# Performance work log

Hardware: AMD Instinct MI355X
Metric: run time of the kernel (lower is better)

Reference implementation:

```python
import jax, jax.numpy as jnp
import numpy as np

N = 32          # agents_num
IN_DIM = 16     # node feature dim (excluding 2 pos cols)
HID = 128
HEADS = 4
OUT = 5
DUEL_H = 256
RADIUS = 0.3
LATENT = HID + HID * HEADS * 2  # 1152
BS = 128


def _lin(k, i, o):
    s = 1.0 / np.sqrt(i)
    return jax.random.uniform(k, (i, o), minval=-s, maxval=s, dtype=jnp.float32)


def setup_inputs() -> dict:
    key = jax.random.key(0)
    ks = jax.random.split(key, 16)
    pos = jax.random.uniform(ks[0], (BS, N, 2))
    feats = jax.random.normal(ks[1], (BS, N, IN_DIM))
    aidx = jax.random.randint(ks[2], (BS,), 0, N).astype(jnp.float32)
    node = jnp.concatenate([pos, feats], axis=-1).reshape(BS, N * (2 + IN_DIM))
    obs = jnp.concatenate([node, aidx[:, None]], axis=1)  # (BS, N*(2+IN_DIM)+1)
    return {
        "obs": obs,
        "enc_w1": _lin(ks[3], IN_DIM, HID), "enc_b1": jnp.zeros((HID,)),
        "enc_w2": _lin(ks[4], HID, HID), "enc_b2": jnp.zeros((HID,)),
        "wl1": _lin(ks[5], HID, HEADS * HID), "wr1": _lin(ks[6], HID, HEADS * HID),
        "att1": jax.random.normal(ks[7], (HEADS, HID)) * 0.1, "bias1": jnp.zeros((HEADS * HID,)),
        "wl2": _lin(ks[8], HID * HEADS, HEADS * HID), "wr2": _lin(ks[9], HID * HEADS, HEADS * HID),
        "att2": jax.random.normal(ks[10], (HEADS, HID)) * 0.1, "bias2": jnp.zeros((HEADS * HID,)),
        "q_w1": _lin(ks[11], LATENT, DUEL_H), "q_b1": jnp.zeros((DUEL_H,)),
        "q_w2": _lin(ks[12], DUEL_H, OUT), "q_b2": jnp.zeros((OUT,)),
        "v_w1": _lin(ks[13], LATENT, DUEL_H), "v_b1": jnp.zeros((DUEL_H,)),
        "v_w2": _lin(ks[14], DUEL_H, 1), "v_b2": jnp.zeros((1,)),
    }


def _gatv2(x, adj, wl, wr, att, bias):
    # Dense-masked GATv2 (PyG semantics: lin_l on source j, lin_r on target i,
    # leaky_relu(x_i + x_j) . att, softmax over neighbors j, aggregate lin_l(x_j)).
    bs, n, _ = x.shape
    gl = (x @ wl).reshape(bs, n, HEADS, HID)  # source transform
    gr = (x @ wr).reshape(bs, n, HEADS, HID)  # target transform
    e = jax.nn.leaky_relu(gr[:, :, None] + gl[:, None, :], 0.2)  # [b, i, j, h, c]
    logits = jnp.einsum('bijhc,hc->bijh', e, att)
    logits = jnp.where(adj[..., None], logits, -jnp.inf)  # diag always True (self loops)
    alpha = jax.nn.softmax(logits, axis=2)
    out = jnp.einsum('bijh,bjhc->bihc', alpha, gl).reshape(bs, n, HEADS * HID)
    return out + bias


def reference(obs, enc_w1, enc_b1, enc_w2, enc_b2,
              wl1, wr1, att1, bias1, wl2, wr2, att2, bias2,
              q_w1, q_b1, q_w2, q_b2, v_w1, v_b1, v_w2, v_b2):
    bs = obs.shape[0]
    node = obs[:, :-1].reshape(bs, N, 2 + IN_DIM)
    pos, feats = node[..., :2], node[..., 2:]
    aidx = jnp.clip(obs[:, -1], 0, N - 1).astype(jnp.int32)

    # radius_graph (per-graph, loop=False) + GATv2 add_self_loops => diag True
    d2 = jnp.sum((pos[:, :, None] - pos[:, None, :]) ** 2, axis=-1)  # [bs, N, N]
    adj = (d2 < RADIUS ** 2) | jnp.eye(N, dtype=bool)

    # encoder MLP then ReLU (as in forward)
    h = jax.nn.relu(feats @ enc_w1 + enc_b1)
    x = jax.nn.relu(h @ enc_w2 + enc_b2)  # [bs, N, HID]

    b = jnp.arange(bs)
    x1 = x[b, aidx]  # [bs, HID]

    x = jax.nn.relu(_gatv2(x, adj, wl1, wr1, att1, bias1))  # [bs, N, HID*HEADS]
    x2 = x[b, aidx]

    x = jax.nn.relu(_gatv2(x, adj, wl2, wr2, att2, bias2))
    x3 = x[b, aidx]

    x_cat = jnp.concatenate([x1, x2, x3], axis=1)  # [bs, LATENT]

    q = jax.nn.relu(x_cat @ q_w1 + q_b1) @ q_w2 + q_b2  # [bs, OUT]
    v = jax.nn.relu(x_cat @ v_w1 + v_b1) @ v_w2 + v_b2  # [bs, 1]
    return q - q.mean(axis=1, keepdims=True) + v
```

## Files before the change

kernel.cpp:

```cpp
#include <hip/hip_runtime.h>
#include <hip/hip_bf16.h>

typedef unsigned int uint_t;
typedef unsigned short ushort_t;
typedef __attribute__((ext_vector_type(8))) short short8;
typedef __attribute__((ext_vector_type(4))) float floatx4;

__device__ __forceinline__ float4 fma4(float4 a, float s, float4 w){
  a.x += s*w.x; a.y += s*w.y; a.z += s*w.z; a.w += s*w.w; return a;
}
__device__ __forceinline__ float4 relu4(float4 a){
  return make_float4(fmaxf(a.x,0.f),fmaxf(a.y,0.f),fmaxf(a.z,0.f),fmaxf(a.w,0.f));
}
__device__ __forceinline__ unsigned bf16rne(float f){
  unsigned u = __float_as_uint(f);
  return (u + 0x7fffu + ((u>>16)&1u)) >> 16;
}
__device__ __forceinline__ uint_t packbf(float f){
  unsigned hb = bf16rne(f);
  float hf = __uint_as_float(hb<<16);
  unsigned lb = bf16rne(f - hf);
  return (hb<<16) | lb;
}
__device__ __forceinline__ uint4 pack4(float4 v){
  uint4 u; u.x=packbf(v.x); u.y=packbf(v.y); u.z=packbf(v.z); u.w=packbf(v.w); return u;
}
__device__ __forceinline__ float unpk(uint_t u){
  return __uint_as_float(u & 0xffff0000u) + __uint_as_float(u<<16);
}
#define UNPACK8(u0,u1,hi,lo) \
  hi[0]=(short)(u0.x>>16); lo[0]=(short)u0.x; \
  hi[1]=(short)(u0.y>>16); lo[1]=(short)u0.y; \
  hi[2]=(short)(u0.z>>16); lo[2]=(short)u0.z; \
  hi[3]=(short)(u0.w>>16); lo[3]=(short)u0.w; \
  hi[4]=(short)(u1.x>>16); lo[4]=(short)u1.x; \
  hi[5]=(short)(u1.y>>16); lo[5]=(short)u1.y; \
  hi[6]=(short)(u1.z>>16); lo[6]=(short)u1.z; \
  hi[7]=(short)(u1.w>>16); lo[7]=(short)u1.w;


__device__ __forceinline__ void hgemm_body(
    const uint_t* __restrict__ xcatpk,
    const ushort_t* __restrict__ qw1Thi, const ushort_t* __restrict__ qw1Tlo,
    const ushort_t* __restrict__ vw1Thi, const ushort_t* __restrict__ vw1Tlo,
    float* __restrict__ part, int ks, int ct, int t)
{
  const int w = t>>6, lane = t&63, m = lane&15, quad = lane>>4;
  const ushort_t* Bhi = (ct<4) ? qw1Thi : vw1Thi;
  const int cbl = (ct<4) ? ct*64 : (ct-4)*64;
  const int cbg = (ct<4) ? ct*64 : 256 + (ct-4)*64;
  const uint_t* ap = xcatpk + (size_t)w*18432 + m*32 + quad*8 + (size_t)(ks*5)*512;
  const ushort_t* bp0 = Bhi + (size_t)((cbl>>4)+0)*18432 + m*32 + quad*8 + (size_t)(ks*5)*512;
  const ushort_t* bp1 = Bhi + (size_t)((cbl>>4)+1)*18432 + m*32 + quad*8 + (size_t)(ks*5)*512;
  const ushort_t* bp2 = Bhi + (size_t)((cbl>>4)+2)*18432 + m*32 + quad*8 + (size_t)(ks*5)*512;
  const ushort_t* bp3 = Bhi + (size_t)((cbl>>4)+3)*18432 + m*32 + quad*8 + (size_t)(ks*5)*512;
  const size_t lod = (size_t)(qw1Tlo - qw1Thi);
  floatx4 acc[4];
  #pragma unroll
  for (int i=0;i<4;i++) acc[i] = (floatx4){0.f,0.f,0.f,0.f};
  #pragma unroll
  for (int kc=0; kc<5; kc++){
    const uint4 ua0 = *(const uint4*)(ap);
    const uint4 ua1 = *(const uint4*)(ap+4);
    ap += 512;
    short8 ahi, alo;
    UNPACK8(ua0,ua1,ahi,alo)
    const ushort_t* bps[4] = {bp0, bp1, bp2, bp3};
    #pragma unroll
    for (int nt=0; nt<4; nt++){
      const short8 bh = *(const short8*)(bps[nt] + kc*512);
      const short8 bl = *(const short8*)(bps[nt] + kc*512 + lod);
      acc[nt] = __builtin_amdgcn_mfma_f32_16x16x32_bf16(ahi, bh, acc[nt], 0,0,0);
      acc[nt] = __builtin_amdgcn_mfma_f32_16x16x32_bf16(ahi, bl, acc[nt], 0,0,0);
      acc[nt] = __builtin_amdgcn_mfma_f32_16x16x32_bf16(alo, bh, acc[nt], 0,0,0);
    }
  }
  float* pdst = part + (size_t)ks*65536;
  const int crow0 = w*16 + quad*4;
  #pragma unroll
  for (int nt=0; nt<4; nt++){
    const int col = cbg + nt*16 + m;
    #pragma unroll
    for (int r=0;r<4;r++)
      pdst[(size_t)(crow0 + r)*512 + col] = acc[nt][r];
  }
}

__global__ __launch_bounds__(256) void prep_kernel(
    const float* __restrict__ obs,
    const float* __restrict__ enc_w1, const float* __restrict__ enc_b1,
    const float* __restrict__ enc_w2, const float* __restrict__ enc_b2,
    const float* __restrict__ wl1, const float* __restrict__ wr1,
    ushort_t* __restrict__ wl1Thi, ushort_t* __restrict__ wl1Tlo,
    ushort_t* __restrict__ wr1Thi, ushort_t* __restrict__ wr1Tlo,
    uint_t* __restrict__ xpk, uint_t* __restrict__ xcatpk,
    unsigned* __restrict__ adjw, int* __restrict__ aiw)
{
  const int t = threadIdx.x, bid = blockIdx.x;
  if (bid >= 512){
    __shared__ float sm[32][33];
    const int cw = bid - 512;
    const float* in; ushort_t* ohi; ushort_t* olo; int tt;
    const int K = 128, N = 512;
    if (cw < 64){ in=wl1; ohi=wl1Thi; olo=wl1Tlo; tt=cw; }
    else        { in=wr1; ohi=wr1Thi; olo=wr1Tlo; tt=cw-64; }
    const int ktiles = K>>5;
    const int kt = tt % ktiles, nt = tt / ktiles;
    const int r = t>>5, c = t&31;
    #pragma unroll
    for (int i=0;i<4;i++)
      sm[r+i*8][c] = in[(size_t)(kt*32 + r + i*8)*N + nt*32 + c];
    __syncthreads();
    #pragma unroll
    for (int i=0;i<4;i++){
      const int nl = r + i*8;
      const int n  = nt*32 + nl;
      const float f = sm[c][nl];
      const unsigned hb = bf16rne(f);
      const float hf = __uint_as_float(hb<<16);
      const unsigned lb = bf16rne(f - hf);
      const size_t off = (size_t)(n>>4)*(16*K) + (size_t)kt*512 + (size_t)(n&15)*32 + c;
      ohi[off] = (ushort_t)hb;
      olo[off] = (ushort_t)lb;
    }
    return;
  }
  __shared__ float s_pos[64];
  __shared__ float s_feats[128];
  __shared__ __align__(16) float s_h[8*132];
  __shared__ int s_ai;
  const int s = bid & 127, g = bid >> 7;
  const float* ob = obs + s*577;

  if (t==0){
    float a = ob[576];
    a = fminf(fmaxf(a, 0.f), 31.f);
    s_ai = (int)a;
    if (g==0) aiw[s] = (int)a;
  }
  if (t < 128){ const int n=t>>4, f=t&15; s_feats[t] = ob[(g*8+n)*18+2+f]; }
  if (g==0 && t>=128 && t<192){ const int u=t-128; s_pos[u] = ob[(u>>1)*18 + (u&1)]; }
  __syncthreads();

  if (g==0 && t < 32){
    const float px = s_pos[2*t], py = s_pos[2*t+1];
    const float R2 = 0.09f;
    unsigned mm = 0u;
    for (int j=0;j<32;j++){
      const float dx = __fsub_rn(px, s_pos[2*j]), dy = __fsub_rn(py, s_pos[2*j+1]);
      const float d2 = __fadd_rn(__fmul_rn(dx,dx), __fmul_rn(dy,dy));
      if (d2 <= R2 || j==t) mm |= (1u<<j);
    }
    adjw[s*32+t] = mm;
  }

  const int n = t>>5, c0 = (t&31)*4;
  {
    float4 a = *(const float4*)(enc_b1+c0);
    #pragma unroll
    for (int f=0; f<16; f++)
      a = fma4(a, s_feats[n*16+f], *(const float4*)(enc_w1 + f*128 + c0));
    *(float4*)&s_h[n*132+c0] = relu4(a);
  }
  __syncthreads();
  {
    float4 a = *(const float4*)(enc_b2+c0);
    for (int k=0;k<128;k+=4){
      const float4 hv = *(const float4*)&s_h[n*132+k];
      a = fma4(a, hv.x, *(const float4*)(enc_w2 + (k+0)*128 + c0));
      a = fma4(a, hv.y, *(const float4*)(enc_w2 + (k+1)*128 + c0));
      a = fma4(a, hv.z, *(const float4*)(enc_w2 + (k+2)*128 + c0));
      a = fma4(a, hv.w, *(const float4*)(enc_w2 + (k+3)*128 + c0));
    }
    a = relu4(a);
    const uint4 p = pack4(a);
    const int i = g*8 + n;
    uint_t* xp = xpk + (size_t)(s*2 + (i>>4))*2048 + (c0>>5)*512 + (i&15)*32 + (c0&31);
    *(uint4*)xp = p;
    if (i == s_ai){
      uint_t* xc = xcatpk + (size_t)(s>>4)*18432 + (c0>>5)*512 + (s&15)*32 + (c0&31);
      *(uint4*)xc = p;
    }
  }
}

__global__ __launch_bounds__(512) void pa1_kernel(
    const uint_t* __restrict__ xpk,
    const ushort_t* __restrict__ wl1Thi, const ushort_t* __restrict__ wl1Tlo,
    const ushort_t* __restrict__ wr1Thi, const ushort_t* __restrict__ wr1Tlo,
    const float* __restrict__ att, const float* __restrict__ bias,
    const unsigned* __restrict__ adjw, const int* __restrict__ aiw,
    const float* __restrict__ wl2, const float* __restrict__ q_w1, const float* __restrict__ v_w1,
    ushort_t* __restrict__ wl2Thi, ushort_t* __restrict__ wl2Tlo,
    ushort_t* __restrict__ qw1Thi, ushort_t* __restrict__ qw1Tlo,
    ushort_t* __restrict__ vw1Thi, ushort_t* __restrict__ vw1Tlo,
    uint_t* __restrict__ x2pk, uint_t* __restrict__ xcatpk)
{
  __shared__ __align__(16) float s_gl[32*132];
  __shared__ __align__(16) float s_glB[32*132];
  __shared__ __align__(16) float s_gr[32*132];
  __shared__ __align__(16) float s_grB[32*132];
  __shared__ __align__(16) float s_att[128];
  __shared__ __align__(16) float s_b[128];
  __shared__ float s_lg[32*33];
  __shared__ unsigned s_adj[32];
  const int t = threadIdx.x, bid = blockIdx.x;

  if (bid >= 512){
    const int cw = bid - 512;
    const float* in; ushort_t* ohi; ushort_t* olo; int K, N, tt;
    if (cw < 256)      { in=wl2;  ohi=wl2Thi; olo=wl2Tlo; K=512;  N=512; tt=cw; }
    else if (cw < 544) { in=q_w1; ohi=qw1Thi; olo=qw1Tlo; K=1152; N=256; tt=cw-256; }
    else               { in=v_w1; ohi=vw1Thi; olo=vw1Tlo; K=1152; N=256; tt=cw-544; }
    const int ktiles = K>>5;
    const int kt = tt % ktiles, nt = tt / ktiles;
    const int r = t>>5, c = t&31;
    #pragma unroll
    for (int i=0;i<2;i++)
      s_gl[(r+i*16)*33 + c] = in[(size_t)(kt*32 + r + i*16)*N + nt*32 + c];
    __syncthreads();
    #pragma unroll
    for (int i=0;i<2;i++){
      const int nl = r + i*16;
      const int n  = nt*32 + nl;
      const float f = s_gl[c*33 + nl];
      const unsigned hb = bf16rne(f);
      const float hf = __uint_as_float(hb<<16);
      const unsigned lb = bf16rne(f - hf);
      const size_t off = (size_t)(n>>4)*(16*K) + (size_t)kt*512 + (size_t)(n&15)*32 + c;
      ohi[off] = (ushort_t)hb;
      olo[off] = (ushort_t)lb;
    }
    return;
  }

  const int s = bid & 127, h = bid >> 7;
  const int w = t>>6, lane = t&63, m = lane&15, quad = lane>>4;
  const int ww = w&3, khalf = w>>2;

  if (t < 128){ s_att[t] = att[h*128 + t]; s_b[t] = bias[h*128 + t]; }
  if (t >= 224 && t < 256) s_adj[t-224] = adjw[s*32 + (t-224)];
  const int ai = aiw[s];

  const ushort_t* Bhi = (ww<2) ? wl1Thi : wr1Thi;
  const ushort_t* Blo = (ww<2) ? wl1Tlo : wr1Tlo;
  const int nbase = h*8 + (ww&1)*4;
  const int kcb = khalf*2;
  const uint_t* a0p = xpk + (size_t)(s*2+0)*2048 + m*32 + quad*8 + kcb*512;
  const uint_t* a1p = xpk + (size_t)(s*2+1)*2048 + m*32 + quad*8 + kcb*512;
  const ushort_t* bp0 = Bhi + (size_t)(nbase+0)*2048 + m*32 + quad*8 + kcb*512;
  const ushort_t* bp1 = Bhi + (size_t)(nbase+1)*2048 + m*32 + quad*8 + kcb*512;
  const ushort_t* bp2 = Bhi + (size_t)(nbase+2)*2048 + m*32 + quad*8 + kcb*512;
  const ushort_t* bp3 = Bhi + (size_t)(nbase+3)*2048 + m*32 + quad*8 + kcb*512;
  const size_t lod = (size_t)(Blo - Bhi);
  floatx4 acc[2][4];
  #pragma unroll
  for (int i=0;i<2;i++)
    #pragma unroll
    for (int j=0;j<4;j++) acc[i][j] = (floatx4){0.f,0.f,0.f,0.f};

  #pragma unroll
  for (int kc=0; kc<2; kc++){
    const uint4 u00 = *(const uint4*)(a0p + kc*512);
    const uint4 u01 = *(const uint4*)(a0p + kc*512 + 4);
    const uint4 u10 = *(const uint4*)(a1p + kc*512);
    const uint4 u11 = *(const uint4*)(a1p + kc*512 + 4);
    short8 ahi0, alo0, ahi1, alo1;
    UNPACK8(u00,u01,ahi0,alo0)
    UNPACK8(u10,u11,ahi1,alo1)
    const ushort_t* bps[4] = {bp0, bp1, bp2, bp3};
    #pragma unroll
    for (int nt=0; nt<4; nt++){
      const short8 bh = *(const short8*)(bps[nt] + kc*512);
      const short8 bl = *(const short8*)(bps[nt] + kc*512 + lod);
      acc[0][nt] = __builtin_amdgcn_mfma_f32_16x16x32_bf16(ahi0, bh, acc[0][nt], 0,0,0);
      acc[0][nt] = __builtin_amdgcn_mfma_f32_16x16x32_bf16(ahi0, bl, acc[0][nt], 0,0,0);
      acc[0][nt] = __builtin_amdgcn_mfma_f32_16x16x32_bf16(alo0, bh, acc[0][nt], 0,0,0);
      acc[1][nt] = __builtin_amdgcn_mfma_f32_16x16x32_bf16(ahi1, bh, acc[1][nt], 0,0,0);
      acc[1][nt] = __builtin_amdgcn_mfma_f32_16x16x32_bf16(ahi1, bl, acc[1][nt], 0,0,0);
      acc[1][nt] = __builtin_amdgcn_mfma_f32_16x16x32_bf16(alo1, bh, acc[1][nt], 0,0,0);
    }
  }
  {
    float* dst = (ww<2) ? (khalf ? s_glB : s_gl) : (khalf ? s_grB : s_gr);
    const int colbase = (ww&1)*64;
    #pragma unroll
    for (int nt=0; nt<4; nt++){
      const int col = colbase + nt*16 + m;
      #pragma unroll
      for (int r=0;r<4;r++){
        dst[(quad*4+r)*132 + col]      = acc[0][nt][r];
        dst[(16+quad*4+r)*132 + col]   = acc[1][nt][r];
      }
    }
  }
  __syncthreads();
  for (int e=t; e<32*132; e+=512){
    s_gl[e] += s_glB[e];
    s_gr[e] += s_grB[e];
  }
  __syncthreads();

  {
    const int i = t>>4, jb = t&15;
    float lacc[2] = {0.f,0.f};
    for (int c=0;c<128;c+=4){
      const float4 g = *(const float4*)&s_gr[i*132+c];
      const float4 a = *(const float4*)&s_att[c];
      #pragma unroll
      for (int mm=0;mm<2;mm++){
        const float4 gj = *(const float4*)&s_gl[(jb+16*mm)*132 + c];
        float ex = g.x+gj.x; ex = fmaxf(ex, 0.2f*ex);
        float ey = g.y+gj.y; ey = fmaxf(ey, 0.2f*ey);
        float ez = g.z+gj.z; ez = fmaxf(ez, 0.2f*ez);
        float ew = g.w+gj.w; ew = fmaxf(ew, 0.2f*ew);
        lacc[mm] += ex*a.x + ey*a.y + ez*a.z + ew*a.w;
      }
    }
    s_lg[i*33 + jb]      = lacc[0];
    s_lg[i*33 + jb + 16] = lacc[1];
  }
  __syncthreads();

  #pragma unroll
  for (int rnd=0; rnd<2; rnd++){
    const int i = rnd*16 + (t>>5), j = t&31;
    const float lg = s_lg[i*33+j];
    const bool ok = (s_adj[i]>>j)&1u;
    float v = ok ? lg : -3.0e38f;
    #pragma unroll
    for (int d_=16; d_; d_>>=1) v = fmaxf(v, __shfl_xor(v, d_, 32));
    const float e = ok ? __expf(lg - v) : 0.f;
    float sum = e;
    #pragma unroll
    for (int d_=16; d_; d_>>=1) sum += __shfl_xor(sum, d_, 32);
    s_lg[i*33+j] = e / sum;
  }
  __syncthreads();

  {
    const int i = t>>4, c0 = (t&15)*8;
    float4 o0 = make_float4(0.f,0.f,0.f,0.f), o1 = o0;
    for (int j=0;j<32;j++){
      const float al = s_lg[i*33+j];
      o0 = fma4(o0, al, *(const float4*)&s_gl[j*132 + c0]);
      o1 = fma4(o1, al, *(const float4*)&s_gl[j*132 + c0 + 4]);
    }
    const float4 b0 = *(const float4*)&s_b[c0];
    const float4 b1 = *(const float4*)&s_b[c0+4];
    o0 = relu4(make_float4(o0.x+b0.x, o0.y+b0.y, o0.z+b0.z, o0.w+b0.w));
    o1 = relu4(make_float4(o1.x+b1.x, o1.y+b1.y, o1.z+b1.z, o1.w+b1.w));
    const uint4 p0 = pack4(o0), p1 = pack4(o1);
    const int kb = h*128 + c0;
    uint_t* xp = x2pk + (size_t)(s*2 + (i>>4))*8192 + (kb>>5)*512 + (i&15)*32 + (kb&31);
    *(uint4*)&xp[0] = p0;
    *(uint4*)&xp[4] = p1;
    if (i == ai){
      const int kk = 128 + kb;
      uint_t* tp = xcatpk + (size_t)(s>>4)*18432 + (kk>>5)*512 + (s&15)*32 + (kk&31);
      *(uint4*)&tp[0] = p0;
      *(uint4*)&tp[4] = p1;
    }
  }
}

__global__ __launch_bounds__(512) void pa2_kernel(
    const uint_t* __restrict__ x2pk,
    const ushort_t* __restrict__ wl2Thi, const ushort_t* __restrict__ wl2Tlo,
    const float* __restrict__ wr2f,
    const float* __restrict__ att2, const float* __restrict__ bias2,
    const unsigned* __restrict__ adjw, const int* __restrict__ aiw,
    const ushort_t* __restrict__ qw1Thi, const ushort_t* __restrict__ qw1Tlo,
    const ushort_t* __restrict__ vw1Thi, const ushort_t* __restrict__ vw1Tlo,
    const float* __restrict__ q_w1f, const float* __restrict__ v_w1f,
    float* __restrict__ hpart, float* __restrict__ hp3,
    uint_t* __restrict__ xcatpk)
{
  const int t = threadIdx.x, bid = blockIdx.x;
  if (bid >= 512){
    const int hk = bid - 512;
    hgemm_body(xcatpk, qw1Thi, qw1Tlo, vw1Thi, vw1Tlo, hpart, hk>>3, hk&7, t);
    return;
  }
  __shared__ __align__(16) float s_gl[32*132];
  __shared__ __align__(16) float s_glB[32*132];
  __shared__ __align__(16) float s_xt[512];
  __shared__ __align__(16) float s_p2[4*128];
  __shared__ __align__(16) float s_at[128];
  __shared__ __align__(16) float s_bb[128];
  __shared__ float s_lg[32];
  __shared__ float s_al[32];
  const int s = bid & 127, h = bid >> 7;
  const int w = t>>6, lane = t&63, m = lane&15, quad = lane>>4;
  const int ww = w&3, khalf = w>>2;
  const int ai = aiw[s];
  const unsigned arow = adjw[s*32+ai];

  {
    const int kk = 128 + t;
    s_xt[t] = unpk(xcatpk[(size_t)(s>>4)*18432 + (kk>>5)*512 + (s&15)*32 + (kk&31)]);
  }
  if (t < 128){ s_at[t] = att2[h*128+t]; s_bb[t] = bias2[h*128+t]; }
  __syncthreads();

  {
    const int c = t&127, q4 = t>>7;
    const float* wp = wr2f + (size_t)(q4*128)*512 + h*128 + c;
    float ga = 0.f;
    #pragma unroll 8
    for (int k=0;k<128;k++) ga += s_xt[q4*128 + k] * wp[(size_t)k*512];
    s_p2[q4*128 + c] = ga;
  }

  const int kcb = khalf*8;
  const uint_t* a0p = x2pk + (size_t)(s*2+0)*8192 + m*32 + quad*8 + kcb*512;
  const uint_t* a1p = x2pk + (size_t)(s*2+1)*8192 + m*32 + quad*8 + kcb*512;
  const ushort_t* bq0 = wl2Thi + (size_t)(h*8 + ww*2+0)*8192 + m*32 + quad*8 + kcb*512;
  const ushort_t* bq1 = wl2Thi + (size_t)(h*8 + ww*2+1)*8192 + m*32 + quad*8 + kcb*512;
  const size_t lod = (size_t)(wl2Tlo - wl2Thi);
  floatx4 acc[2][2];
  #pragma unroll
  for (int i=0;i<2;i++){ acc[i][0] = (floatx4){0.f,0.f,0.f,0.f}; acc[i][1] = acc[i][0]; }
  #pragma unroll 4
  for (int kc=0; kc<8; kc++){
    const uint4 u00 = *(const uint4*)(a0p + kc*512);
    const uint4 u01 = *(const uint4*)(a0p + kc*512 + 4);
    const uint4 u10 = *(const uint4*)(a1p + kc*512);
    const uint4 u11 = *(const uint4*)(a1p + kc*512 + 4);
    short8 ahi0, alo0, ahi1, alo1;
    UNPACK8(u00,u01,ahi0,alo0)
    UNPACK8(u10,u11,ahi1,alo1)
    {
      const short8 bh = *(const short8*)(bq0 + kc*512);
      const short8 bl = *(const short8*)(bq0 + kc*512 + lod);
      acc[0][0] = __builtin_amdgcn_mfma_f32_16x16x32_bf16(ahi0, bh, acc[0][0], 0,0,0);
      acc[0][0] = __builtin_amdgcn_mfma_f32_16x16x32_bf16(ahi0, bl, acc[0][0], 0,0,0);
      acc[0][0] = __builtin_amdgcn_mfma_f32_16x16x32_bf16(alo0, bh, acc[0][0], 0,0,0);
      acc[1][0] = __builtin_amdgcn_mfma_f32_16x16x32_bf16(ahi1, bh, acc[1][0], 0,0,0);
      acc[1][0] = __builtin_amdgcn_mfma_f32_16x16x32_bf16(ahi1, bl, acc[1][0], 0,0,0);
      acc[1][0] = __builtin_amdgcn_mfma_f32_16x16x32_bf16(alo1, bh, acc[1][0], 0,0,0);
    }
    {
      const short8 bh = *(const short8*)(bq1 + kc*512);
      const short8 bl = *(const short8*)(bq1 + kc*512 + lod);
      acc[0][1] = __builtin_amdgcn_mfma_f32_16x16x32_bf16(ahi0, bh, acc[0][1], 0,0,0);
      acc[0][1] = __builtin_amdgcn_mfma_f32_16x16x32_bf16(ahi0, bl, acc[0][1], 0,0,0);
      acc[0][1] = __builtin_amdgcn_mfma_f32_16x16x32_bf16(alo0, bh, acc[0][1], 0,0,0);
      acc[1][1] = __builtin_amdgcn_mfma_f32_16x16x32_bf16(ahi1, bh, acc[1][1], 0,0,0);
      acc[1][1] = __builtin_amdgcn_mfma_f32_16x16x32_bf16(ahi1, bl, acc[1][1], 0,0,0);
      acc[1][1] = __builtin_amdgcn_mfma_f32_16x16x32_bf16(alo1, bh, acc[1][1], 0,0,0);
    }
  }
  {
    float* dst = khalf ? s_glB : s_gl;
    const int colbase = ww*32;
    #pragma unroll
    for (int nt=0; nt<2; nt++){
      const int col = colbase + nt*16 + m;
      #pragma unroll
      for (int r=0;r<4;r++){
        dst[(quad*4+r)*132 + col]    = acc[0][nt][r];
        dst[(16+quad*4+r)*132 + col] = acc[1][nt][r];
      }
    }
  }
  __syncthreads();
  for (int e=t; e<32*132; e+=512) s_gl[e] += s_glB[e];
  if (t < 128) s_p2[t] = s_p2[t] + s_p2[128+t] + s_p2[256+t] + s_p2[384+t];
  __syncthreads();

  if (t < 256){
    const int j = t>>3, pq = t&7;
    float sum = 0.f;
    #pragma unroll
    for (int q=0;q<4;q++){
      const int c = pq*16 + q*4;
      const float4 g = *(const float4*)&s_gl[j*132 + c];
      const float4 r = *(const float4*)&s_p2[c];
      const float4 a = *(const float4*)&s_at[c];
      float e0 = r.x+g.x; e0 = fmaxf(e0, 0.2f*e0);
      float e1 = r.y+g.y; e1 = fmaxf(e1, 0.2f*e1);
      float e2 = r.z+g.z; e2 = fmaxf(e2, 0.2f*e2);
      float e3 = r.w+g.w; e3 = fmaxf(e3, 0.2f*e3);
      sum += e0*a.x + e1*a.y + e2*a.z + e3*a.w;
    }
    sum += __shfl_xor(sum,1,64);
    sum += __shfl_xor(sum,2,64);
    sum += __shfl_xor(sum,4,64);
    if (pq==0) s_lg[j] = sum;
  }
  __syncthreads();
  if (t < 32){
    const float lg = s_lg[t];
    const bool ok = (arow>>t)&1u;
    float v = ok ? lg : -3.0e38f;
    #pragma unroll
    for (int d_=16; d_; d_>>=1) v = fmaxf(v, __shfl_xor(v, d_, 32));
    const float e = ok ? __expf(lg - v) : 0.f;
    float sm = e;
    #pragma unroll
    for (int d_=16; d_; d_>>=1) sm += __shfl_xor(sm, d_, 32);
    s_al[t] = e / sm;
  }
  __syncthreads();
  if (t < 128){
    float acc2 = 0.f;
    #pragma unroll 8
    for (int j=0;j<32;j++) acc2 += s_al[j] * s_gl[j*132 + t];
    const float x3v = fmaxf(acc2 + s_bb[t], 0.f);
    const int kk = 640 + h*128 + t;
    xcatpk[(size_t)(s>>4)*18432 + (kk>>5)*512 + (s&15)*32 + (kk&31)] = packbf(x3v);
    s_xt[t] = x3v;
  }
  __syncthreads();

  {
    const float* W; int col;
    if (t < 256){ W = q_w1f; col = t; }
    else        { W = v_w1f; col = t-256; }
    const float* wp = W + (size_t)(640 + h*128)*256 + col;
    float acc3 = 0.f;
    #pragma unroll 8
    for (int k=0;k<128;k++) acc3 += s_xt[k] * wp[(size_t)k*256];
    hp3[((size_t)h*128 + s)*512 + t] = acc3;
  }
}

__global__ __launch_bounds__(256) void hepi_kernel(
    const float* __restrict__ hpart, const float* __restrict__ hp3,
    const float* __restrict__ q_b1, const float* __restrict__ q_w2, const float* __restrict__ q_b2,
    const float* __restrict__ v_b1, const float* __restrict__ v_w2, const float* __restrict__ v_b2,
    float* __restrict__ out)
{
  __shared__ float s_p[4*6];
  const int t = threadIdx.x, s = blockIdx.x;
  float hq = q_b1[t], hv = v_b1[t];
  #pragma unroll
  for (int ks=0; ks<4; ks++){
    hq += hpart[(size_t)ks*65536 + (size_t)s*512 + t];
    hv += hpart[(size_t)ks*65536 + (size_t)s*512 + 256 + t];
  }
  #pragma unroll
  for (int h=0; h<4; h++){
    hq += hp3[((size_t)h*128 + s)*512 + t];
    hv += hp3[((size_t)h*128 + s)*512 + 256 + t];
  }
  hq = fmaxf(hq, 0.f);
  hv = fmaxf(hv, 0.f);
  float p[6];
  #pragma unroll
  for (int o=0;o<5;o++) p[o] = hq * q_w2[t*5+o];
  p[5] = hv * v_w2[t];
  #pragma unroll
  for (int d_=32; d_; d_>>=1){
    #pragma unroll
    for (int o=0;o<6;o++) p[o] += __shfl_xor(p[o], d_, 64);
  }
  const int w = t>>6, lane = t&63;
  if (lane==0){
    #pragma unroll
    for (int o=0;o<6;o++) s_p[w*6+o] = p[o];
  }
  __syncthreads();
  if (t < 6) s_p[t] = s_p[t] + s_p[6+t] + s_p[12+t] + s_p[18+t];
  __syncthreads();
  if (t < 5){
    const float q0 = s_p[0]+q_b2[0], q1 = s_p[1]+q_b2[1], q2 = s_p[2]+q_b2[2],
                q3 = s_p[3]+q_b2[3], q4 = s_p[4]+q_b2[4];
    const float mean = (q0+q1+q2+q3+q4) / 5.0f;
    const float v = s_p[5] + v_b2[0];
    const float qt = (t==0?q0:t==1?q1:t==2?q2:t==3?q3:q4);
    out[s*5+t] = qt - mean + v;
  }
}

extern "C" void kernel_launch(void* const* d_in, const int* in_sizes, int n_in,
                              void* d_out, int out_size, void* d_ws, size_t ws_size,
                              hipStream_t stream) {
  (void)n_in; (void)out_size; (void)ws_size;
  const float* obs    = (const float*)d_in[0];
  const float* enc_w1 = (const float*)d_in[1];
  const float* enc_b1 = (const float*)d_in[2];
  const float* enc_w2 = (const float*)d_in[3];
  const float* enc_b2 = (const float*)d_in[4];
  const float* wl1    = (const float*)d_in[5];
  const float* wr1    = (const float*)d_in[6];
  const float* att1   = (const float*)d_in[7];
  const float* bias1  = (const float*)d_in[8];
  const float* wl2    = (const float*)d_in[9];
  const float* wr2    = (const float*)d_in[10];
  const float* att2   = (const float*)d_in[11];
  const float* bias2  = (const float*)d_in[12];
  const float* q_w1   = (const float*)d_in[13];
  const float* q_b1   = (const float*)d_in[14];
  const float* q_w2   = (const float*)d_in[15];
  const float* q_b2   = (const float*)d_in[16];
  const float* v_w1   = (const float*)d_in[17];
  const float* v_b1   = (const float*)d_in[18];
  const float* v_w2   = (const float*)d_in[19];
  const float* v_b2   = (const float*)d_in[20];

  char* ws = (char*)d_ws;
  uint_t*   x_pk    = (uint_t*)  (ws + 0);
  uint_t*   xcat_pk = (uint_t*)  (ws + 2097152);
  unsigned* adjw    = (unsigned*)(ws + 2686976);
  int*      aiw     = (int*)     (ws + 2703360);
  uint_t*   x2_pk   = (uint_t*)  (ws + 2703872);
  ushort_t* wl1Thi  = (ushort_t*)(ws + 11092480);
  ushort_t* wl1Tlo  = (ushort_t*)(ws + 11223552);
  ushort_t* wr1Thi  = (ushort_t*)(ws + 11354624);
  ushort_t* wr1Tlo  = (ushort_t*)(ws + 11485696);
  ushort_t* wl2Thi  = (ushort_t*)(ws + 11616768);
  ushort_t* wl2Tlo  = (ushort_t*)(ws + 12141056);
  ushort_t* qw1Thi  = (ushort_t*)(ws + 12665344);
  ushort_t* qw1Tlo  = (ushort_t*)(ws + 13255168);
  ushort_t* vw1Thi  = (ushort_t*)(ws + 13844992);
  ushort_t* vw1Tlo  = (ushort_t*)(ws + 14434816);
  float*    hpart   = (float*)   (ws + 15024640);
  float*    hp3     = (float*)   (ws + 16073216);

  const int bs = in_sizes[0] / 577;

  prep_kernel<<<512 + 128, 256, 0, stream>>>(obs, enc_w1, enc_b1, enc_w2, enc_b2,
      wl1, wr1, wl1Thi, wl1Tlo, wr1Thi, wr1Tlo,
      x_pk, xcat_pk, adjw, aiw);

  pa1_kernel<<<512 + 832, 512, 0, stream>>>(x_pk, wl1Thi, wl1Tlo, wr1Thi, wr1Tlo,
      att1, bias1, adjw, aiw,
      wl2, q_w1, v_w1, wl2Thi, wl2Tlo, qw1Thi, qw1Tlo, vw1Thi, vw1Tlo,
      x2_pk, xcat_pk);

  pa2_kernel<<<512 + 32, 512, 0, stream>>>(x2_pk, wl2Thi, wl2Tlo, wr2,
      att2, bias2, adjw, aiw,
      qw1Thi, qw1Tlo, vw1Thi, vw1Tlo, q_w1, v_w1, hpart, hp3, xcat_pk);

  hepi_kernel<<<bs, 256, 0, stream>>>(hpart, hp3, q_b1, q_w2, q_b2, v_b1, v_w2, v_b2,
                                      (float*)d_out);
}
```

Before: 176.7 us.

## Move layer-2 target transform and x3 dueling GEMM to split-bf16 MFMA kernels

Adds a gr2 kernel that computes the layer-2 target transform of the agent rows as a split-bf16 MFMA GEMM. The wr2 pre-split is done in the pa1 conversion blocks, and the first part of the dueling-head GEMM runs alongside in the same kernel. The x3 contribution to the dueling hidden layer is moved out of pa2's scalar FP32 loop into a new MFMA kernel that writes extra partial slots into hpart. pa1 and pa2 change their MFMA work split so each wave covers the full K range, which removes the double shared buffers and the reduction pass. The cost is two extra kernel launches and hpart now sharing workspace with x_pk.

```diff
diff --git a/kernel.cpp b/kernel.cpp
--- a/kernel.cpp
+++ b/kernel.cpp
@@ -39,27 +39,29 @@
   hi[7]=(short)(u1.w>>16); lo[7]=(short)u1.w;
 
 
+template<int NKC>
 __device__ __forceinline__ void hgemm_body(
     const uint_t* __restrict__ xcatpk,
     const ushort_t* __restrict__ qw1Thi, const ushort_t* __restrict__ qw1Tlo,
     const ushort_t* __restrict__ vw1Thi, const ushort_t* __restrict__ vw1Tlo,
-    float* __restrict__ part, int ks, int ct, int t)
+    float* __restrict__ part, int ks, int ct, int t, int k0c, int slot0)
 {
   const int w = t>>6, lane = t&63, m = lane&15, quad = lane>>4;
   const ushort_t* Bhi = (ct<4) ? qw1Thi : vw1Thi;
   const int cbl = (ct<4) ? ct*64 : (ct-4)*64;
   const int cbg = (ct<4) ? ct*64 : 256 + (ct-4)*64;
-  const uint_t* ap = xcatpk + (size_t)w*18432 + m*32 + quad*8 + (size_t)(ks*5)*512;
-  const ushort_t* bp0 = Bhi + (size_t)((cbl>>4)+0)*18432 + m*32 + quad*8 + (size_t)(ks*5)*512;
-  const ushort_t* bp1 = Bhi + (size_t)((cbl>>4)+1)*18432 + m*32 + quad*8 + (size_t)(ks*5)*512;
-  const ushort_t* bp2 = Bhi + (size_t)((cbl>>4)+2)*18432 + m*32 + quad*8 + (size_t)(ks*5)*512;
-  const ushort_t* bp3 = Bhi + (size_t)((cbl>>4)+3)*18432 + m*32 + quad*8 + (size_t)(ks*5)*512;
+  const int kb = k0c + ks*NKC;
+  const uint_t* ap = xcatpk + (size_t)w*18432 + m*32 + quad*8 + (size_t)kb*512;
+  const ushort_t* bp0 = Bhi + (size_t)((cbl>>4)+0)*18432 + m*32 + quad*8 + (size_t)kb*512;
+  const ushort_t* bp1 = Bhi + (size_t)((cbl>>4)+1)*18432 + m*32 + quad*8 + (size_t)kb*512;
+  const ushort_t* bp2 = Bhi + (size_t)((cbl>>4)+2)*18432 + m*32 + quad*8 + (size_t)kb*512;
+  const ushort_t* bp3 = Bhi + (size_t)((cbl>>4)+3)*18432 + m*32 + quad*8 + (size_t)kb*512;
   const size_t lod = (size_t)(qw1Tlo - qw1Thi);
   floatx4 acc[4];
   #pragma unroll
   for (int i=0;i<4;i++) acc[i] = (floatx4){0.f,0.f,0.f,0.f};
   #pragma unroll
-  for (int kc=0; kc<5; kc++){
+  for (int kc=0; kc<NKC; kc++){
     const uint4 ua0 = *(const uint4*)(ap);
     const uint4 ua1 = *(const uint4*)(ap+4);
     ap += 512;
@@ -75,7 +77,7 @@
       acc[nt] = __builtin_amdgcn_mfma_f32_16x16x32_bf16(alo, bh, acc[nt], 0,0,0);
     }
   }
-  float* pdst = part + (size_t)ks*65536;
+  float* pdst = part + (size_t)(slot0+ks)*65536;
   const int crow0 = w*16 + quad*4;
   #pragma unroll
   for (int nt=0; nt<4; nt++){
@@ -190,16 +192,16 @@
     const ushort_t* __restrict__ wr1Thi, const ushort_t* __restrict__ wr1Tlo,
     const float* __restrict__ att, const float* __restrict__ bias,
     const unsigned* __restrict__ adjw, const int* __restrict__ aiw,
-    const float* __restrict__ wl2, const float* __restrict__ q_w1, const float* __restrict__ v_w1,
+    const float* __restrict__ wl2, const float* __restrict__ q_w1,
+    const float* __restrict__ v_w1, const float* __restrict__ wr2,
     ushort_t* __restrict__ wl2Thi, ushort_t* __restrict__ wl2Tlo,
     ushort_t* __restrict__ qw1Thi, ushort_t* __restrict__ qw1Tlo,
     ushort_t* __restrict__ vw1Thi, ushort_t* __restrict__ vw1Tlo,
+    ushort_t* __restrict__ wr2Thi, ushort_t* __restrict__ wr2Tlo,
     uint_t* __restrict__ x2pk, uint_t* __restrict__ xcatpk)
 {
   __shared__ __align__(16) float s_gl[32*132];
-  __shared__ __align__(16) float s_glB[32*132];
   __shared__ __align__(16) float s_gr[32*132];
-  __shared__ __align__(16) float s_grB[32*132];
   __shared__ __align__(16) float s_att[128];
   __shared__ __align__(16) float s_b[128];
   __shared__ float s_lg[32*33];
@@ -211,7 +213,8 @@
     const float* in; ushort_t* ohi; ushort_t* olo; int K, N, tt;
     if (cw < 256)      { in=wl2;  ohi=wl2Thi; olo=wl2Tlo; K=512;  N=512; tt=cw; }
     else if (cw < 544) { in=q_w1; ohi=qw1Thi; olo=qw1Tlo; K=1152; N=256; tt=cw-256; }
-    else               { in=v_w1; ohi=vw1Thi; olo=vw1Tlo; K=1152; N=256; tt=cw-544; }
+    else if (cw < 832) { in=v_w1; ohi=vw1Thi; olo=vw1Tlo; K=1152; N=256; tt=cw-544; }
+    else               { in=wr2;  ohi=wr2Thi; olo=wr2Tlo; K=512;  N=512; tt=cw-832; }
     const int ktiles = K>>5;
     const int kt = tt % ktiles, nt = tt / ktiles;
     const int r = t>>5, c = t&31;
@@ -236,31 +239,28 @@
 
   const int s = bid & 127, h = bid >> 7;
   const int w = t>>6, lane = t&63, m = lane&15, quad = lane>>4;
-  const int ww = w&3, khalf = w>>2;
+  const int mat = w>>2, cpair = w&3;
 
   if (t < 128){ s_att[t] = att[h*128 + t]; s_b[t] = bias[h*128 + t]; }
   if (t >= 224 && t < 256) s_adj[t-224] = adjw[s*32 + (t-224)];
   const int ai = aiw[s];
 
-  const ushort_t* Bhi = (ww<2) ? wl1Thi : wr1Thi;
-  const ushort_t* Blo = (ww<2) ? wl1Tlo : wr1Tlo;
-  const int nbase = h*8 + (ww&1)*4;
-  const int kcb = khalf*2;
-  const uint_t* a0p = xpk + (size_t)(s*2+0)*2048 + m*32 + quad*8 + kcb*512;
-  const uint_t* a1p = xpk + (size_t)(s*2+1)*2048 + m*32 + quad*8 + kcb*512;
-  const ushort_t* bp0 = Bhi + (size_t)(nbase+0)*2048 + m*32 + quad*8 + kcb*512;
-  const ushort_t* bp1 = Bhi + (size_t)(nbase+1)*2048 + m*32 + quad*8 + kcb*512;
-  const ushort_t* bp2 = Bhi + (size_t)(nbase+2)*2048 + m*32 + quad*8 + kcb*512;
-  const ushort_t* bp3 = Bhi + (size_t)(nbase+3)*2048 + m*32 + quad*8 + kcb*512;
+  const ushort_t* Bhi = (mat==0) ? wl1Thi : wr1Thi;
+  const ushort_t* Blo = (mat==0) ? wl1Tlo : wr1Tlo;
+  const int nbase = h*8 + cpair*2;
+  const uint_t* a0p = xpk + (size_t)(s*2+0)*2048 + m*32 + quad*8;
+  const uint_t* a1p = xpk + (size_t)(s*2+1)*2048 + m*32 + quad*8;
+  const ushort_t* bp0 = Bhi + (size_t)(nbase+0)*2048 + m*32 + quad*8;
+  const ushort_t* bp1 = Bhi + (size_t)(nbase+1)*2048 + m*32 + quad*8;
   const size_t lod = (size_t)(Blo - Bhi);
-  floatx4 acc[2][4];
+  floatx4 acc[2][2];
   #pragma unroll
   for (int i=0;i<2;i++)
     #pragma unroll
-    for (int j=0;j<4;j++) acc[i][j] = (floatx4){0.f,0.f,0.f,0.f};
-
-  #pragma unroll
-  for (int kc=0; kc<2; kc++){
+    for (int j=0;j<2;j++) acc[i][j] = (floatx4){0.f,0.f,0.f,0.f};
+
+  #pragma unroll
+  for (int kc=0; kc<4; kc++){
     const uint4 u00 = *(const uint4*)(a0p + kc*512);
     const uint4 u01 = *(const uint4*)(a0p + kc*512 + 4);
     const uint4 u10 = *(const uint4*)(a1p + kc*512);
@@ -268,9 +268,9 @@
     short8 ahi0, alo0, ahi1, alo1;
     UNPACK8(u00,u01,ahi0,alo0)
     UNPACK8(u10,u11,ahi1,alo1)
-    const ushort_t* bps[4] = {bp0, bp1, bp2, bp3};
-    #pragma unroll
-    for (int nt=0; nt<4; nt++){
+    const ushort_t* bps[2] = {bp0, bp1};
+    #pragma unroll
+    for (int nt=0; nt<2; nt++){
       const short8 bh = *(const short8*)(bps[nt] + kc*512);
       const short8 bl = *(const short8*)(bps[nt] + kc*512 + lod);
       acc[0][nt] = __builtin_amdgcn_mfma_f32_16x16x32_bf16(ahi0, bh, acc[0][nt], 0,0,0);
@@ -282,10 +282,10 @@
     }
   }
   {
-    float* dst = (ww<2) ? (khalf ? s_glB : s_gl) : (khalf ? s_grB : s_gr);
-    const int colbase = (ww&1)*64;
-    #pragma unroll
-    for (int nt=0; nt<4; nt++){
+    float* dst = mat ? s_gr : s_gl;
+    const int colbase = cpair*32;
+    #pragma unroll
+    for (int nt=0; nt<2; nt++){
       const int col = colbase + nt*16 + m;
       #pragma unroll
       for (int r=0;r<4;r++){
@@ -293,11 +293,6 @@
         dst[(16+quad*4+r)*132 + col]   = acc[1][nt][r];
       }
     }
-  }
-  __syncthreads();
-  for (int e=t; e<32*132; e+=512){
-    s_gl[e] += s_glB[e];
-    s_gr[e] += s_grB[e];
   }
   __syncthreads();
 
@@ -364,65 +359,77 @@
   }
 }
 
+__global__ __launch_bounds__(512) void gr2_kernel(
+    const uint_t* __restrict__ xcatpk,
+    const ushort_t* __restrict__ wr2Thi, const ushort_t* __restrict__ wr2Tlo,
+    const ushort_t* __restrict__ qw1Thi, const ushort_t* __restrict__ qw1Tlo,
+    const ushort_t* __restrict__ vw1Thi, const ushort_t* __restrict__ vw1Tlo,
+    float* __restrict__ hpart, float* __restrict__ GR)
+{
+  const int t = threadIdx.x, bid = blockIdx.x;
+  if (bid >= 32){
+    const int hk = bid - 32;
+    hgemm_body<5>(xcatpk, qw1Thi, qw1Tlo, vw1Thi, vw1Tlo, hpart, hk>>3, hk&7, t, 0, 0);
+    return;
+  }
+  const int w = t>>6, lane = t&63, m = lane&15, quad = lane>>4;
+  const int rt = w;
+  const int ctl = bid;
+  const uint_t* ap = xcatpk + (size_t)rt*18432 + m*32 + quad*8 + (size_t)4*512;
+  const ushort_t* bp = wr2Thi + (size_t)ctl*8192 + m*32 + quad*8;
+  const size_t lod = (size_t)(wr2Tlo - wr2Thi);
+  floatx4 acc = (floatx4){0.f,0.f,0.f,0.f};
+  #pragma unroll 4
+  for (int kc=0; kc<16; kc++){
+    const uint4 ua0 = *(const uint4*)(ap + kc*512);
+    const uint4 ua1 = *(const uint4*)(ap + kc*512 + 4);
+    short8 ahi, alo;
+    UNPACK8(ua0,ua1,ahi,alo)
+    const short8 bh = *(const short8*)(bp + kc*512);
+    const short8 bl = *(const short8*)(bp + kc*512 + lod);
+    acc = __builtin_amdgcn_mfma_f32_16x16x32_bf16(ahi, bh, acc, 0,0,0);
+    acc = __builtin_amdgcn_mfma_f32_16x16x32_bf16(ahi, bl, acc, 0,0,0);
+    acc = __builtin_amdgcn_mfma_f32_16x16x32_bf16(alo, bh, acc, 0,0,0);
+  }
+  const int row0 = rt*16 + quad*4, col = ctl*16 + m;
+  #pragma unroll
+  for (int r=0;r<4;r++)
+    GR[(size_t)(row0 + r)*512 + col] = acc[r];
+}
+
 __global__ __launch_bounds__(512) void pa2_kernel(
     const uint_t* __restrict__ x2pk,
     const ushort_t* __restrict__ wl2Thi, const ushort_t* __restrict__ wl2Tlo,
-    const float* __restrict__ wr2f,
+    const float* __restrict__ GR,
     const float* __restrict__ att2, const float* __restrict__ bias2,
     const unsigned* __restrict__ adjw, const int* __restrict__ aiw,
-    const ushort_t* __restrict__ qw1Thi, const ushort_t* __restrict__ qw1Tlo,
-    const ushort_t* __restrict__ vw1Thi, const ushort_t* __restrict__ vw1Tlo,
-    const float* __restrict__ q_w1f, const float* __restrict__ v_w1f,
-    float* __restrict__ hpart, float* __restrict__ hp3,
     uint_t* __restrict__ xcatpk)
 {
-  const int t = threadIdx.x, bid = blockIdx.x;
-  if (bid >= 512){
-    const int hk = bid - 512;
-    hgemm_body(xcatpk, qw1Thi, qw1Tlo, vw1Thi, vw1Tlo, hpart, hk>>3, hk&7, t);
-    return;
-  }
   __shared__ __align__(16) float s_gl[32*132];
-  __shared__ __align__(16) float s_glB[32*132];
-  __shared__ __align__(16) float s_xt[512];
-  __shared__ __align__(16) float s_p2[4*128];
+  __shared__ __align__(16) float s_p2[128];
   __shared__ __align__(16) float s_at[128];
   __shared__ __align__(16) float s_bb[128];
   __shared__ float s_lg[32];
   __shared__ float s_al[32];
+  const int t = threadIdx.x, bid = blockIdx.x;
   const int s = bid & 127, h = bid >> 7;
   const int w = t>>6, lane = t&63, m = lane&15, quad = lane>>4;
-  const int ww = w&3, khalf = w>>2;
   const int ai = aiw[s];
   const unsigned arow = adjw[s*32+ai];
 
-  {
-    const int kk = 128 + t;
-    s_xt[t] = unpk(xcatpk[(size_t)(s>>4)*18432 + (kk>>5)*512 + (s&15)*32 + (kk&31)]);
-  }
-  if (t < 128){ s_at[t] = att2[h*128+t]; s_bb[t] = bias2[h*128+t]; }
-  __syncthreads();
-
-  {
-    const int c = t&127, q4 = t>>7;
-    const float* wp = wr2f + (size_t)(q4*128)*512 + h*128 + c;
-    float ga = 0.f;
-    #pragma unroll 8
-    for (int k=0;k<128;k++) ga += s_xt[q4*128 + k] * wp[(size_t)k*512];
-    s_p2[q4*128 + c] = ga;
-  }
-
-  const int kcb = khalf*8;
-  const uint_t* a0p = x2pk + (size_t)(s*2+0)*8192 + m*32 + quad*8 + kcb*512;
-  const uint_t* a1p = x2pk + (size_t)(s*2+1)*8192 + m*32 + quad*8 + kcb*512;
-  const ushort_t* bq0 = wl2Thi + (size_t)(h*8 + ww*2+0)*8192 + m*32 + quad*8 + kcb*512;
-  const ushort_t* bq1 = wl2Thi + (size_t)(h*8 + ww*2+1)*8192 + m*32 + quad*8 + kcb*512;
+  if (t < 128){
+    s_p2[t] = GR[(size_t)s*512 + h*128 + t];
+    s_at[t] = att2[h*128+t];
+    s_bb[t] = bias2[h*128+t];
+  }
+
+  const uint_t* a0p = x2pk + (size_t)(s*2+0)*8192 + m*32 + quad*8;
+  const uint_t* a1p = x2pk + (size_t)(s*2+1)*8192 + m*32 + quad*8;
+  const ushort_t* bq = wl2Thi + (size_t)(h*8 + w)*8192 + m*32 + quad*8;
   const size_t lod = (size_t)(wl2Tlo - wl2Thi);
-  floatx4 acc[2][2];
-  #pragma unroll
-  for (int i=0;i<2;i++){ acc[i][0] = (floatx4){0.f,0.f,0.f,0.f}; acc[i][1] = acc[i][0]; }
+  floatx4 acc0 = (floatx4){0.f,0.f,0.f,0.f}, acc1 = acc0;
   #pragma unroll 4
-  for (int kc=0; kc<8; kc++){
+  for (int kc=0; kc<16; kc++){
     const uint4 u00 = *(const uint4*)(a0p + kc*512);
     const uint4 u01 = *(const uint4*)(a0p + kc*512 + 4);
     const uint4 u10 = *(const uint4*)(a1p + kc*512);
@@ -430,43 +437,23 @@
     short8 ahi0, alo0, ahi1, alo1;
     UNPACK8(u00,u01,ahi0,alo0)
     UNPACK8(u10,u11,ahi1,alo1)
-    {
-      const short8 bh = *(const short8*)(bq0 + kc*512);
-      const short8 bl = *(const short8*)(bq0 + kc*512 + lod);
-      acc[0][0] = __builtin_amdgcn_mfma_f32_16x16x32_bf16(ahi0, bh, acc[0][0], 0,0,0);
-      acc[0][0] = __builtin_amdgcn_mfma_f32_16x16x32_bf16(ahi0, bl, acc[0][0], 0,0,0);
-      acc[0][0] = __builtin_amdgcn_mfma_f32_16x16x32_bf16(alo0, bh, acc[0][0], 0,0,0);
-      acc[1][0] = __builtin_amdgcn_mfma_f32_16x16x32_bf16(ahi1, bh, acc[1][0], 0,0,0);
-      acc[1][0] = __builtin_amdgcn_mfma_f32_16x16x32_bf16(ahi1, bl, acc[1][0], 0,0,0);
-      acc[1][0] = __builtin_amdgcn_mfma_f32_16x16x32_bf16(alo1, bh, acc[1][0], 0,0,0);
-    }
-    {
-      const short8 bh = *(const short8*)(bq1 + kc*512);
-      const short8 bl = *(const short8*)(bq1 + kc*512 + lod);
-      acc[0][1] = __builtin_amdgcn_mfma_f32_16x16x32_bf16(ahi0, bh, acc[0][1], 0,0,0);
-      acc[0][1] = __builtin_amdgcn_mfma_f32_16x16x32_bf16(ahi0, bl, acc[0][1], 0,0,0);
-      acc[0][1] = __builtin_amdgcn_mfma_f32_16x16x32_bf16(alo0, bh, acc[0][1], 0,0,0);
-      acc[1][1] = __builtin_amdgcn_mfma_f32_16x16x32_bf16(ahi1, bh, acc[1][1], 0,0,0);
-      acc[1][1] = __builtin_amdgcn_mfma_f32_16x16x32_bf16(ahi1, bl, acc[1][1], 0,0,0);
-      acc[1][1] = __builtin_amdgcn_mfma_f32_16x16x32_bf16(alo1, bh, acc[1][1], 0,0,0);
-    }
+    const short8 bh = *(const short8*)(bq + kc*512);
+    const short8 bl = *(const short8*)(bq + kc*512 + lod);
+    acc0 = __builtin_amdgcn_mfma_f32_16x16x32_bf16(ahi0, bh, acc0, 0,0,0);
+    acc0 = __builtin_amdgcn_mfma_f32_16x16x32_bf16(ahi0, bl, acc0, 0,0,0);
+    acc0 = __builtin_amdgcn_mfma_f32_16x16x32_bf16(alo0, bh, acc0, 0,0,0);
+    acc1 = __builtin_amdgcn_mfma_f32_16x16x32_bf16(ahi1, bh, acc1, 0,0,0);
+    acc1 = __builtin_amdgcn_mfma_f32_16x16x32_bf16(ahi1, bl, acc1, 0,0,0);
+    acc1 = __builtin_amdgcn_mfma_f32_16x16x32_bf16(alo1, bh, acc1, 0,0,0);
   }
   {
-    float* dst = khalf ? s_glB : s_gl;
-    const int colbase = ww*32;
-    #pragma unroll
-    for (int nt=0; nt<2; nt++){
-      const int col = colbase + nt*16 + m;
-      #pragma unroll
-      for (int r=0;r<4;r++){
-        dst[(quad*4+r)*132 + col]    = acc[0][nt][r];
-        dst[(16+quad*4+r)*132 + col] = acc[1][nt][r];
-      }
-    }
-  }
-  __syncthreads();
-  for (int e=t; e<32*132; e+=512) s_gl[e] += s_glB[e];
-  if (t < 128) s_p2[t] = s_p2[t] + s_p2[128+t] + s_p2[256+t] + s_p2[384+t];
+    const int col = w*16 + m;
+    #pragma unroll
+    for (int r=0;r<4;r++){
+      s_gl[(quad*4+r)*132 + col]    = acc0[r];
+      s_gl[(16+quad*4+r)*132 + col] = acc1[r];
+    }
+  }
   __syncthreads();
 
   if (t < 256){
@@ -510,24 +497,21 @@
     const float x3v = fmaxf(acc2 + s_bb[t], 0.f);
     const int kk = 640 + h*128 + t;
     xcatpk[(size_t)(s>>4)*18432 + (kk>>5)*512 + (s&15)*32 + (kk&31)] = packbf(x3v);
-    s_xt[t] = x3v;
-  }
-  __syncthreads();
-
-  {
-    const float* W; int col;
-    if (t < 256){ W = q_w1f; col = t; }
-    else        { W = v_w1f; col = t-256; }
-    const float* wp = W + (size_t)(640 + h*128)*256 + col;
-    float acc3 = 0.f;
-    #pragma unroll 8
-    for (int k=0;k<128;k++) acc3 += s_xt[k] * wp[(size_t)k*256];
-    hp3[((size_t)h*128 + s)*512 + t] = acc3;
-  }
+  }
+}
+
+__global__ __launch_bounds__(512) void x3g_kernel(
+    const uint_t* __restrict__ xcatpk,
+    const ushort_t* __restrict__ qw1Thi, const ushort_t* __restrict__ qw1Tlo,
+    const ushort_t* __restrict__ vw1Thi, const ushort_t* __restrict__ vw1Tlo,
+    float* __restrict__ hpart)
+{
+  const int t = threadIdx.x, bid = blockIdx.x;
+  hgemm_body<4>(xcatpk, qw1Thi, qw1Tlo, vw1Thi, vw1Tlo, hpart, bid>>3, bid&7, t, 20, 4);
 }
 
 __global__ __launch_bounds__(256) void hepi_kernel(
-    const float* __restrict__ hpart, const float* __restrict__ hp3,
+    const float* __restrict__ hpart,
     const float* __restrict__ q_b1, const float* __restrict__ q_w2, const float* __restrict__ q_b2,
     const float* __restrict__ v_b1, const float* __restrict__ v_w2, const float* __restrict__ v_b2,
     float* __restrict__ out)
@@ -536,14 +520,9 @@
   const int t = threadIdx.x, s = blockIdx.x;
   float hq = q_b1[t], hv = v_b1[t];
   #pragma unroll
-  for (int ks=0; ks<4; ks++){
+  for (int ks=0; ks<8; ks++){
     hq += hpart[(size_t)ks*65536 + (size_t)s*512 + t];
     hv += hpart[(size_t)ks*65536 + (size_t)s*512 + 256 + t];
-  }
-  #pragma unroll
-  for (int h=0; h<4; h++){
-    hq += hp3[((size_t)h*128 + s)*512 + t];
-    hv += hp3[((size_t)h*128 + s)*512 + 256 + t];
   }
   hq = fmaxf(hq, 0.f);
   hv = fmaxf(hv, 0.f);
@@ -602,6 +581,7 @@
 
   char* ws = (char*)d_ws;
   uint_t*   x_pk    = (uint_t*)  (ws + 0);
+  float*    hpart   = (float*)   (ws + 0);
   uint_t*   xcat_pk = (uint_t*)  (ws + 2097152);
   unsigned* adjw    = (unsigned*)(ws + 2686976);
   int*      aiw     = (int*)     (ws + 2703360);
@@ -616,24 +596,31 @@
   ushort_t* qw1Tlo  = (ushort_t*)(ws + 13255168);
   ushort_t* vw1Thi  = (ushort_t*)(ws + 13844992);
   ushort_t* vw1Tlo  = (ushort_t*)(ws + 14434816);
-  float*    hpart   = (float*)   (ws + 15024640);
-  float*    hp3     = (float*)   (ws + 16073216);
+  ushort_t* wr2Thi  = (ushort_t*)(ws + 15024640);
+  ushort_t* wr2Tlo  = (ushort_t*)(ws + 15548928);
+  float*    GR      = (float*)   (ws + 16073216);
 
   const int bs = in_sizes[0] / 577;
+  (void)bs;
 
   prep_kernel<<<512 + 128, 256, 0, stream>>>(obs, enc_w1, enc_b1, enc_w2, enc_b2,
       wl1, wr1, wl1Thi, wl1Tlo, wr1Thi, wr1Tlo,
       x_pk, xcat_pk, adjw, aiw);
 
-  pa1_kernel<<<512 + 832, 512, 0, stream>>>(x_pk, wl1Thi, wl1Tlo, wr1Thi, wr1Tlo,
+  pa1_kernel<<<512 + 1088, 512, 0, stream>>>(x_pk, wl1Thi, wl1Tlo, wr1Thi, wr1Tlo,
       att1, bias1, adjw, aiw,
-      wl2, q_w1, v_w1, wl2Thi, wl2Tlo, qw1Thi, qw1Tlo, vw1Thi, vw1Tlo,
+      wl2, q_w1, v_w1, wr2,
+      wl2Thi, wl2Tlo, qw1Thi, qw1Tlo, vw1Thi, vw1Tlo, wr2Thi, wr2Tlo,
       x2_pk, xcat_pk);
 
-  pa2_kernel<<<512 + 32, 512, 0, stream>>>(x2_pk, wl2Thi, wl2Tlo, wr2,
-      att2, bias2, adjw, aiw,
-      qw1Thi, qw1Tlo, vw1Thi, vw1Tlo, q_w1, v_w1, hpart, hp3, xcat_pk);
-
-  hepi_kernel<<<bs, 256, 0, stream>>>(hpart, hp3, q_b1, q_w2, q_b2, v_b1, v_w2, v_b2,
-                                      (float*)d_out);
-}
+  gr2_kernel<<<64, 512, 0, stream>>>(xcat_pk, wr2Thi, wr2Tlo,
+      qw1Thi, qw1Tlo, vw1Thi, vw1Tlo, hpart, GR);
+
+  pa2_kernel<<<512, 512, 0, stream>>>(x2_pk, wl2Thi, wl2Tlo, GR,
+      att2, bias2, adjw, aiw, xcat_pk);
+
+  x3g_kernel<<<32, 512, 0, stream>>>(xcat_pk, qw1Thi, qw1Tlo, vw1Thi, vw1Tlo, hpart);
+
+  hepi_kernel<<<128, 256, 0, stream>>>(hpart, q_b1, q_w2, q_b2, v_b1, v_w2, v_b2,
+                                       (float*)d_out);
+}
```

Measured after the change: 197.0 us. 11.5% more time.
